# Kernel optimization log

Measured on AMD Instinct MI355X. Metric: run time of the kernel, lower is better.

Reference implementation:

```python
import jax, jax.numpy as jnp
import numpy as np

B, S, D, L, H = 2, 2048, 2048, 3, 16
DH = D // H
BLOCK = 16
NA = 64
Q = NA * BLOCK
KV = S + Q
VOCAB = 32000
MASK_ID = 31999
GAMMA = 7.0
EPS = 1e-6


def _rope(x, pos):
    # x: [B,H,T,DH], pos: [B,T]
    half = DH // 2
    inv = 1.0 / (10000.0 ** (jnp.arange(half, dtype=jnp.float32) / half))
    ang = pos[:, None, :, None].astype(jnp.float32) * inv  # [B,1,T,half]
    c, s = jnp.cos(ang), jnp.sin(ang)
    x1, x2 = x[..., :half], x[..., half:]
    return jnp.concatenate([x1 * c - x2 * s, x2 * c + x1 * s], axis=-1)


def setup_inputs() -> dict:
    key = jax.random.key(0)
    ks = jax.random.split(key, 12)
    w = lambda k, shp: 0.02 * jax.random.normal(k, shp, jnp.float32)
    return {
        'input_ids': jax.random.randint(ks[0], (B, S), 0, VOCAB, dtype=jnp.int32),
        'hidden_states': jax.random.normal(ks[1], (L, B, S, D), jnp.float32),
        'loss_mask': jnp.ones((B, S), jnp.int32),
        'lm_head_weight': w(ks[2], (VOCAB, D)),
        'norm_weight': jnp.ones((D,), jnp.float32),
        'anchor_positions': jnp.sort(jax.random.randint(ks[3], (B, NA), 0, S - BLOCK, dtype=jnp.int32), axis=-1),
        'ctx_proj_w': w(ks[4], (D, L * D)),
        'embed_table': w(ks[5], (VOCAB, D)),
        'wq': w(ks[6], (D, D)),
        'wk': w(ks[7], (D, D)),
        'wv': w(ks[8], (D, D)),
        'wo': w(ks[9], (D, D)),
    }


def reference(input_ids, hidden_states, loss_mask, lm_head_weight, norm_weight,
              anchor_positions, ctx_proj_w, embed_table, wq, wk, wv, wo):
    # --- context feature: concat L target-layer hiddens, project to D ---
    ctx_cat = jnp.transpose(hidden_states, (1, 2, 0, 3)).reshape(B, S, L * D)
    ctx = jnp.einsum('bsf,df->bsd', ctx_cat, ctx_proj_w)

    # --- position ids (context: 0..S-1; draft block i starts at anchor_i) ---
    ctx_pos = jnp.broadcast_to(jnp.arange(S, dtype=jnp.int32), (B, S))
    draft_pos = (anchor_positions[:, :, None] + jnp.arange(BLOCK, dtype=jnp.int32)[None, None, :]).reshape(B, Q)

    # --- draft input (anchor token + MASKs) and labels ---
    off = jnp.arange(Q, dtype=jnp.int32) % BLOCK                       # [Q]
    anchor_per_tok = jnp.repeat(anchor_positions, BLOCK, axis=1)       # [B,Q]
    anchor_tok = jnp.take_along_axis(input_ids, anchor_positions, axis=1)
    draft_ids = jnp.where(off[None, :] == 0, jnp.repeat(anchor_tok, BLOCK, axis=1), MASK_ID)
    labels = jnp.where(off[None, :] == 0, -100,
                       jnp.take_along_axis(input_ids, anchor_per_tok + off[None, :], axis=1))

    # --- block-causal mask: [B,Q,KV] ---
    qi = jnp.arange(Q, dtype=jnp.int32)
    ki = jnp.arange(KV, dtype=jnp.int32)
    qb = qi // BLOCK                                                   # [Q]
    apos = anchor_positions[:, qb]                                     # [B,Q]
    ctx_vis = (ki[None, None, :] < S) & (ki[None, None, :] < apos[:, :, None])
    kb = (ki - S) // BLOCK
    draft_vis = (ki >= S)[None, :] & (qb[:, None] == kb[None, :])      # [Q,KV]
    mask = ctx_vis | draft_vis[None]                                   # [B,Q,KV]

    # --- single RoPE attention layer: draft queries over [context; draft] ---
    emb = embed_table[draft_ids]                                       # [B,Q,D]
    x_kv = jnp.concatenate([ctx, emb], axis=1)                         # [B,KV,D]
    pos_kv = jnp.concatenate([ctx_pos, draft_pos], axis=1)             # [B,KV]
    q = _rope((emb @ wq.T).reshape(B, Q, H, DH).transpose(0, 2, 1, 3), draft_pos)
    k = _rope((x_kv @ wk.T).reshape(B, KV, H, DH).transpose(0, 2, 1, 3), pos_kv)
    v = (x_kv @ wv.T).reshape(B, KV, H, DH).transpose(0, 2, 1, 3)
    scores = jnp.einsum('bhqd,bhkd->bhqk', q, k) / np.float32(np.sqrt(DH))
    scores = jnp.where(mask[:, None], scores, jnp.float32(-1e30))
    attn = jax.nn.softmax(scores, axis=-1)
    out = jnp.einsum('bhqk,bhkd->bhqd', attn, v).transpose(0, 2, 1, 3).reshape(B, Q, D) @ wo.T
    hidden = emb + out

    # --- RMSNorm + LM head ---
    hidden = hidden * jax.lax.rsqrt(jnp.mean(hidden * hidden, -1, keepdims=True) + EPS) * norm_weight
    logits = hidden @ lm_head_weight.T                                 # [B,Q,VOCAB]

    # --- decay-weighted CE loss + accuracy ---
    logp = jax.nn.log_softmax(logits, axis=-1)
    lab = jnp.where(labels < 0, 0, labels)
    nll = -jnp.take_along_axis(logp, lab[..., None], axis=-1)[..., 0]
    valid = labels != -100
    offf = off.astype(jnp.float32)
    decay = jnp.where(off == 0, 0.0, jnp.exp(-(offf - 1.0) / GAMMA))   # [Q]
    w = decay[None, :] * valid.astype(jnp.float32)
    loss = jnp.sum(nll * w) / jnp.maximum(jnp.sum(w), 1e-6)
    preds = jnp.argmax(logits, axis=-1).astype(labels.dtype)
    acc = jnp.sum((preds == labels) & valid) / jnp.maximum(jnp.sum(valid), 1)
    return loss, acc.astype(jnp.float32)
```

## Files before the change

kernel.cpp:

```cpp
#include <hip/hip_runtime.h>

#define B_ 2
#define S_ 2048
#define D_ 2048
#define L_ 3
#define H_ 16
#define DH_ 128
#define BLK_ 16
#define NA_ 64
#define Q_ 1024
#define KV_ 3072
#define VOCAB_ 32000
#define MASK_ID_ 31999
#define NTOK_ (B_*Q_)
#define VTILES_ (VOCAB_/128)
#define NCHUNK_ 4

typedef __attribute__((ext_vector_type(8))) short bf16x8;
typedef __attribute__((ext_vector_type(4))) float f32x4;
typedef const __attribute__((address_space(1))) void* gptr_t;
typedef __attribute__((address_space(3))) void* lptr_t;

__device__ inline unsigned short f2bf(float x) {
  unsigned int u = __float_as_uint(x);
  unsigned int r = (u + 0x7fff + ((u >> 16) & 1)) >> 16;
  return (unsigned short)r;
}
__device__ inline float bf2f(unsigned short u) {
  return __uint_as_float(((unsigned int)u) << 16);
}

__global__ void k_meta(const int* __restrict__ ids, const int* __restrict__ anchors,
                       int* __restrict__ dids, int* __restrict__ dpos, int* __restrict__ labels) {
  int t = blockIdx.x * 256 + threadIdx.x;
  if (t >= NTOK_) return;
  int b = t >> 10, qi = t & 1023;
  int a = qi >> 4, off = qi & 15;
  int ap = anchors[b * NA_ + a];
  dpos[t] = ap + off;
  dids[t] = (off == 0) ? ids[b * S_ + ap] : MASK_ID_;
  labels[t] = (off == 0) ? -100 : ids[b * S_ + ap + off];
}

__global__ void k_cvt(const float* __restrict__ in, unsigned short* __restrict__ out, int n4) {
  int i = blockIdx.x * 256 + threadIdx.x;
  if (i >= n4) return;
  float4 v = ((const float4*)in)[i];
  ushort4 o;
  o.x = f2bf(v.x); o.y = f2bf(v.y); o.z = f2bf(v.z); o.w = f2bf(v.w);
  ((ushort4*)out)[i] = o;
}

__global__ void k_cvt_ctx(const float* __restrict__ hs, unsigned short* __restrict__ out) {
  int bi = blockIdx.x;
  int l = bi % 3, row = bi / 3;
  const float4* src = (const float4*)(hs + ((size_t)l * B_ * S_ + row) * (size_t)D_);
  ushort4* dst = (ushort4*)(out + (size_t)row * (3 * D_) + (size_t)l * D_);
  for (int i = threadIdx.x; i < D_ / 4; i += 256) {
    float4 v = src[i];
    ushort4 o;
    o.x = f2bf(v.x); o.y = f2bf(v.y); o.z = f2bf(v.z); o.w = f2bf(v.w);
    dst[i] = o;
  }
}

__global__ void k_gather(const float* __restrict__ table, const int* __restrict__ dids,
                         unsigned short* __restrict__ x_kv) {
  int row = blockIdx.x;
  int b = row >> 10, qi = row & 1023;
  const float4* src = (const float4*)(table + (size_t)dids[row] * D_);
  ushort4* dst = (ushort4*)(x_kv + ((size_t)b * KV_ + S_ + qi) * D_);
  for (int i = threadIdx.x; i < D_ / 4; i += 256) {
    float4 v = src[i];
    ushort4 o;
    o.x = f2bf(v.x); o.y = f2bf(v.y); o.z = f2bf(v.z); o.w = f2bf(v.w);
    dst[i] = o;
  }
}

template <int CMODE, int MAP>
__global__ __launch_bounds__(256) void k_mfma_bt(
    const unsigned short* __restrict__ A, const unsigned short* __restrict__ Bw,
    float* __restrict__ Cf, unsigned short* __restrict__ Cb,
    int M, int N, int K, int adivlog, long long abump, int cdivlog, long long cbump,
    const int* __restrict__ labels, float* __restrict__ pm, float* __restrict__ ps,
    int* __restrict__ pbi, float* __restrict__ plab) {
  __shared__ unsigned short As[128 * 32];
  __shared__ unsigned short Bs[128 * 32];
  int bx, by;
  if (MAP == 0) {
    int ntn = N >> 7;
    bx = blockIdx.x % ntn, by = blockIdx.x / ntn;
  } else {
    int per = gridDim.x >> 3;
    int wgid = (blockIdx.x & 7) * per + (blockIdx.x >> 3);
    int ntm = M >> 7;
    by = wgid % ntm, bx = wgid / ntm;
  }
  int rowbase = by << 7, colbase = bx << 7;
  int tid = threadIdx.x, lane = tid & 63, w = tid >> 6;
  int wr = w >> 1, wc = w & 1;
  int lo = lane & 15, hi = lane >> 4;

  f32x4 acc[4][4];
#pragma unroll
  for (int m = 0; m < 4; ++m)
#pragma unroll
    for (int n = 0; n < 4; ++n) acc[m][n] = (f32x4){0.f, 0.f, 0.f, 0.f};

  for (int kt = 0; kt < K; kt += 32) {
#pragma unroll
    for (int i = 0; i < 2; ++i) {
      int seg = i * 4 + w;
      int rloc = seg * 16 + (lane >> 2);
      int kcol = kt + ((lane & 3) << 3);
      int ra = rowbase + rloc;
      long long aoff = (long long)ra * K + (long long)(ra >> adivlog) * abump + kcol;
      __builtin_amdgcn_global_load_lds((gptr_t)(A + aoff), (lptr_t)(As + seg * 512), 16, 0, 0);
      int rb = colbase + rloc;
      long long boff = (long long)rb * K + kcol;
      __builtin_amdgcn_global_load_lds((gptr_t)(Bw + boff), (lptr_t)(Bs + seg * 512), 16, 0, 0);
    }
    __syncthreads();
    bf16x8 af[4], bfv[4];
#pragma unroll
    for (int m = 0; m < 4; ++m) {
      int row = wr * 64 + m * 16 + lo;
      af[m] = *(const bf16x8*)(As + row * 32 + (hi << 3));
    }
#pragma unroll
    for (int n = 0; n < 4; ++n) {
      int row = wc * 64 + n * 16 + lo;
      bfv[n] = *(const bf16x8*)(Bs + row * 32 + (hi << 3));
    }
#pragma unroll
    for (int m = 0; m < 4; ++m)
#pragma unroll
      for (int n = 0; n < 4; ++n)
        acc[m][n] = __builtin_amdgcn_mfma_f32_16x16x32_bf16(af[m], bfv[n], acc[m][n], 0, 0, 0);
    __syncthreads();
  }

  if (CMODE == 0 || CMODE == 1) {
#pragma unroll
    for (int m = 0; m < 4; ++m)
#pragma unroll
      for (int n = 0; n < 4; ++n)
#pragma unroll
        for (int r4 = 0; r4 < 4; ++r4) {
          int row = rowbase + wr * 64 + m * 16 + hi * 4 + r4;
          int col = colbase + wc * 64 + n * 16 + lo;
          size_t addr = (size_t)row * N + (size_t)(row >> cdivlog) * cbump + col;
          if (CMODE == 0) Cf[addr] = acc[m][n][r4];
          else Cb[addr] = f2bf(acc[m][n][r4]);
        }
  } else if (CMODE == 3) {
#pragma unroll
    for (int m = 0; m < 4; ++m)
#pragma unroll
      for (int n = 0; n < 4; ++n)
#pragma unroll
        for (int r4 = 0; r4 < 4; ++r4) {
          int row = rowbase + wr * 64 + m * 16 + hi * 4 + r4;
          int col = colbase + wc * 64 + n * 16 + lo;
          int bb = row >= KV_;
          int kv = row - bb * KV_;
          size_t addr = ((size_t)(bb * H_ + (col >> 7)) * 128 + (col & 127)) * KV_ + kv;
          Cb[addr] = f2bf(acc[m][n][r4]);
        }
  } else {
    float* f = (float*)As;
    int* ii = (int*)Bs;
    if (tid < 128) { f[640 + tid] = -3.0e38f; ii[256 + tid] = labels[rowbase + tid]; }
    __syncthreads();
#pragma unroll
    for (int m = 0; m < 4; ++m)
#pragma unroll
      for (int r4 = 0; r4 < 4; ++r4) {
        int trow = wr * 64 + m * 16 + hi * 4 + r4;
        float mx = acc[m][0][r4];
        int arg = colbase + wc * 64 + 0 * 16 + lo;
#pragma unroll
        for (int n = 1; n < 4; ++n) {
          float v = acc[m][n][r4];
          int c = colbase + wc * 64 + n * 16 + lo;
          if (v > mx || (v == mx && c < arg)) { mx = v; arg = c; }
        }
#pragma unroll
        for (int d = 1; d < 16; d <<= 1) {
          float om = __shfl_xor(mx, d);
          int oc = __shfl_xor(arg, d);
          if (om > mx || (om == mx && oc < arg)) { mx = om; arg = oc; }
        }
        if (lo == 0) { f[wc * 128 + trow] = mx; ii[wc * 128 + trow] = arg; }
      }
    __syncthreads();
    if (tid < 128) {
      float a = f[tid], b = f[128 + tid];
      int aa = ii[tid], bb = ii[128 + tid];
      float g; int ga;
      if (b > a || (b == a && bb < aa)) { g = b; ga = bb; } else { g = a; ga = aa; }
      f[512 + tid] = g; ii[384 + tid] = ga;
    }
    __syncthreads();
#pragma unroll
    for (int m = 0; m < 4; ++m)
#pragma unroll
      for (int r4 = 0; r4 < 4; ++r4) {
        int trow = wr * 64 + m * 16 + hi * 4 + r4;
        float gm = f[512 + trow];
        float s = 0.f;
#pragma unroll
        for (int n = 0; n < 4; ++n) s += __expf(acc[m][n][r4] - gm);
#pragma unroll
        for (int d = 1; d < 16; d <<= 1) s += __shfl_xor(s, d);
        if (lo == 0) f[256 + wc * 128 + trow] = s;
        int lab = ii[256 + trow];
        int rel = lab - colbase - wc * 64;
        if (rel >= 0 && rel < 64 && (rel & 15) == lo) {
#pragma unroll
          for (int n = 0; n < 4; ++n)
            if ((rel >> 4) == n) f[640 + trow] = acc[m][n][r4];
        }
      }
    __syncthreads();
    if (tid < 128) {
      int grow = rowbase + tid;
      size_t p = (size_t)grow * VTILES_ + bx;
      pm[p] = f[512 + tid];
      ps[p] = f[256 + tid] + f[256 + 128 + tid];
      pbi[p] = ii[384 + tid];
      plab[p] = f[640 + tid];
    }
  }
}

__global__ void k_rope(unsigned short* __restrict__ x, const int* __restrict__ dpos, int mode) {
  int idx = blockIdx.x * 256 + threadIdx.x;
  int j = idx & 63;
  int h = (idx >> 6) & 15;
  int row = idx >> 10;
  int pos;
  if (mode == 0) {
    if (row >= NTOK_) return;
    pos = dpos[row];
  } else {
    if (row >= B_ * KV_) return;
    int b = row / KV_, kvi = row % KV_;
    pos = (kvi < S_) ? kvi : dpos[b * Q_ + (kvi - S_)];
  }
  float inv = expf(-(float)j * (9.210340371976184f / 64.f));
  float ang = (float)pos * inv;
  float c = cosf(ang), s = sinf(ang);
  unsigned short* p = x + (size_t)row * D_ + h * DH_ + j;
  float x1 = bf2f(p[0]), x2 = bf2f(p[64]);
  p[0] = f2bf(x1 * c - x2 * s);
  p[64] = f2bf(x2 * c + x1 * s);
}

__global__ __launch_bounds__(256) void k_attn_part(
    const unsigned short* __restrict__ qb, const unsigned short* __restrict__ kb,
    const unsigned short* __restrict__ vt, const int* __restrict__ anchors,
    float* __restrict__ pm_att, float* __restrict__ pl_att, float* __restrict__ po_att) {
  __shared__ __align__(16) unsigned short P_all[4][16 * 40];
  int w = threadIdx.x >> 6, lane = threadIdx.x & 63;
  int blk = blockIdx.x * 4 + w;
  int chunk = blk & 3, h = (blk >> 2) & 15, a = (blk >> 6) & 63, b = blk >> 12;
  int ql = lane & 15, p = lane >> 4;
  int apos = anchors[b * NA_ + a];

  int cstart = chunk << 9;
  int cend = min(apos, cstart + 512);
  int len = (cend > cstart) ? (cend - cstart) : 0;
  int ntile = (len + 31) >> 5;
  int total = ntile + ((chunk == 3) ? 1 : 0);

  if (total == 0) {
    if (p == 0) { pm_att[blk * 16 + ql] = -3.0e38f; pl_att[blk * 16 + ql] = 0.f; }
    return;
  }
  unsigned short* P = P_all[w];

  const unsigned short* qbase = qb + ((size_t)(b * Q_ + a * 16 + ql)) * D_ + h * DH_;
  bf16x8 qf[4];
#pragma unroll
  for (int ks = 0; ks < 4; ++ks)
    qf[ks] = *(const bf16x8*)(qbase + ks * 32 + p * 8);

  const unsigned short* kbb = kb + (size_t)b * KV_ * D_ + h * DH_;
  const unsigned short* vtb = vt + ((size_t)(b * H_ + h)) * 128 * KV_;

  f32x4 o[8];
#pragma unroll
  for (int nt = 0; nt < 8; ++nt) o[nt] = (f32x4){0.f, 0.f, 0.f, 0.f};
  float mrun = -3.0e38f, lrun = 0.f;
  const float scl = 0.08838834764831845f;

  for (int t = 0; t < total; ++t) {
    bool isdraft = (chunk == 3) && (t == ntile);
    int ktb = isdraft ? (S_ + a * 16) : (cstart + (t << 5));
    int vc = isdraft ? 16 : min(32, cend - ktb);
    float s[2][4];
#pragma unroll
    for (int g = 0; g < 2; ++g) {
      if (g * 16 < vc) {
        f32x4 accs = (f32x4){0.f, 0.f, 0.f, 0.f};
        const unsigned short* krow = kbb + (size_t)(ktb + g * 16 + ql) * D_;
#pragma unroll
        for (int ks = 0; ks < 4; ++ks) {
          bf16x8 kf = *(const bf16x8*)(krow + ks * 32 + p * 8);
          accs = __builtin_amdgcn_mfma_f32_16x16x32_bf16(kf, qf[ks], accs, 0, 0, 0);
        }
#pragma unroll
        for (int r = 0; r < 4; ++r) {
          int kl = g * 16 + p * 4 + r;
          s[g][r] = (kl < vc) ? accs[r] * scl : -3.0e38f;
        }
      } else {
#pragma unroll
        for (int r = 0; r < 4; ++r) s[g][r] = -3.0e38f;
      }
    }
    float mt = s[0][0];
#pragma unroll
    for (int g = 0; g < 2; ++g)
#pragma unroll
      for (int r = 0; r < 4; ++r) mt = fmaxf(mt, s[g][r]);
    mt = fmaxf(mt, __shfl_xor(mt, 16));
    mt = fmaxf(mt, __shfl_xor(mt, 32));
    float mnew = fmaxf(mrun, mt);
    float corr = __expf(mrun - mnew);
    float psum = 0.f;
#pragma unroll
    for (int g = 0; g < 2; ++g) {
      float p0 = __expf(s[g][0] - mnew), p1 = __expf(s[g][1] - mnew);
      float p2 = __expf(s[g][2] - mnew), p3 = __expf(s[g][3] - mnew);
      psum += p0 + p1 + p2 + p3;
      ushort2 w0, w1;
      w0.x = f2bf(p0); w0.y = f2bf(p1); w1.x = f2bf(p2); w1.y = f2bf(p3);
      int eo = ql * 40 + g * 16 + p * 4;
      *(ushort2*)(P + eo) = w0;
      *(ushort2*)(P + eo + 2) = w1;
    }
    psum += __shfl_xor(psum, 16);
    psum += __shfl_xor(psum, 32);
    lrun = lrun * corr + psum;
    mrun = mnew;
    float cr[4];
#pragma unroll
    for (int r = 0; r < 4; ++r) cr[r] = __shfl(corr, p * 4 + r);
#pragma unroll
    for (int nt = 0; nt < 8; ++nt)
#pragma unroll
      for (int r = 0; r < 4; ++r) o[nt][r] *= cr[r];
    bf16x8 pf = *(const bf16x8*)(P + ql * 40 + p * 8);
#pragma unroll
    for (int nt = 0; nt < 8; ++nt) {
      bf16x8 vf = *(const bf16x8*)(vtb + (size_t)(nt * 16 + ql) * KV_ + ktb + p * 8);
      o[nt] = __builtin_amdgcn_mfma_f32_16x16x32_bf16(pf, vf, o[nt], 0, 0, 0);
    }
  }
  if (p == 0) { pm_att[blk * 16 + ql] = mrun; pl_att[blk * 16 + ql] = lrun; }
  float* pob = po_att + (size_t)blk * 2048;
#pragma unroll
  for (int nt = 0; nt < 8; ++nt)
#pragma unroll
    for (int r = 0; r < 4; ++r)
      pob[(p * 4 + r) * 128 + nt * 16 + ql] = o[nt][r];
}

__global__ __launch_bounds__(256) void k_attn_combine(
    const float* __restrict__ pm_att, const float* __restrict__ pl_att,
    const float* __restrict__ po_att, unsigned short* __restrict__ ob) {
  int base = blockIdx.x;
  int h = base & 15, a = (base >> 4) & 63, b = base >> 10;
  int d = threadIdx.x & 127, qh = threadIdx.x >> 7;
  int pbase = base * 4;
#pragma unroll
  for (int qq = 0; qq < 8; ++qq) {
    int q = qh * 8 + qq;
    float m0 = pm_att[(pbase + 0) * 16 + q], m1 = pm_att[(pbase + 1) * 16 + q];
    float m2 = pm_att[(pbase + 2) * 16 + q], m3 = pm_att[(pbase + 3) * 16 + q];
    float mg = fmaxf(fmaxf(m0, m1), fmaxf(m2, m3));
    float w0 = __expf(m0 - mg), w1 = __expf(m1 - mg);
    float w2 = __expf(m2 - mg), w3 = __expf(m3 - mg);
    float lg = pl_att[(pbase + 0) * 16 + q] * w0 + pl_att[(pbase + 1) * 16 + q] * w1 +
               pl_att[(pbase + 2) * 16 + q] * w2 + pl_att[(pbase + 3) * 16 + q] * w3;
    float od = po_att[(size_t)(pbase + 0) * 2048 + q * 128 + d] * w0 +
               po_att[(size_t)(pbase + 1) * 2048 + q * 128 + d] * w1 +
               po_att[(size_t)(pbase + 2) * 2048 + q * 128 + d] * w2 +
               po_att[(size_t)(pbase + 3) * 2048 + q * 128 + d] * w3;
    ob[((size_t)(b * Q_ + a * 16 + q)) * D_ + h * DH_ + d] = f2bf(od / lg);
  }
}

__global__ void k_rmsnorm(const unsigned short* __restrict__ x_kv, const float* __restrict__ proj,
                          const float* __restrict__ nw, unsigned short* __restrict__ outp) {
  int row = blockIdx.x;
  int b = row >> 10, qi = row & 1023;
  const unsigned short* emb = x_kv + ((size_t)b * KV_ + S_ + qi) * D_;
  const float* pr = proj + (size_t)row * D_;
  __shared__ float red[256];
  float h[8];
  float ssum = 0.f;
#pragma unroll
  for (int i = 0; i < 8; ++i) {
    int d = threadIdx.x + i * 256;
    h[i] = bf2f(emb[d]) + pr[d];
    ssum += h[i] * h[i];
  }
  red[threadIdx.x] = ssum;
  __syncthreads();
  for (int s = 128; s; s >>= 1) {
    if (threadIdx.x < s) red[threadIdx.x] += red[threadIdx.x + s];
    __syncthreads();
  }
  float scale = rsqrtf(red[0] / (float)D_ + 1e-6f);
#pragma unroll
  for (int i = 0; i < 8; ++i) {
    int d = threadIdx.x + i * 256;
    outp[(size_t)row * D_ + d] = f2bf(h[i] * scale * nw[d]);
  }
}

__global__ void k_combine(const float* __restrict__ pm, const float* __restrict__ ps,
                          const int* __restrict__ pbi, const float* __restrict__ plab,
                          const int* __restrict__ labels, float* __restrict__ ts) {
  int t = blockIdx.x * 256 + threadIdx.x;
  if (t >= NTOK_) return;
  const float* pmr = pm + (size_t)t * VTILES_;
  const float* psr = ps + (size_t)t * VTILES_;
  const int* pbir = pbi + (size_t)t * VTILES_;
  const float* plabr = plab + (size_t)t * VTILES_;
  float M = -3.0e38f; int bi = 0;
  for (int x = 0; x < VTILES_; ++x) {
    float v = pmr[x];
    if (v > M) { M = v; bi = pbir[x]; }
  }
  float ssum = 0.f, labl = -3.0e38f;
  for (int x = 0; x < VTILES_; ++x) {
    ssum += psr[x] * __expf(pmr[x] - M);
    labl = fmaxf(labl, plabr[x]);
  }
  float lse = M + logf(ssum);
  int lab = labels[t];
  int off = t & 15;
  float valid = (lab != -100) ? 1.f : 0.f;
  float w = (off == 0) ? 0.f : __expf(-(float)(off - 1) / 7.0f);
  w *= valid;
  float nll = (lab != -100) ? (lse - labl) : 0.f;
  float correct = (valid > 0.f && bi == lab) ? 1.f : 0.f;
  ts[t * 4 + 0] = nll * w;
  ts[t * 4 + 1] = w;
  ts[t * 4 + 2] = correct;
  ts[t * 4 + 3] = valid;
}

__global__ void k_finalize(const float* __restrict__ ts, float* __restrict__ out) {
  __shared__ float r0[256], r1[256], r2[256], r3[256];
  int tid = threadIdx.x;
  float s0 = 0, s1 = 0, s2 = 0, s3 = 0;
  for (int t = tid; t < NTOK_; t += 256) {
    s0 += ts[t * 4 + 0]; s1 += ts[t * 4 + 1];
    s2 += ts[t * 4 + 2]; s3 += ts[t * 4 + 3];
  }
  r0[tid] = s0; r1[tid] = s1; r2[tid] = s2; r3[tid] = s3;
  __syncthreads();
  for (int s = 128; s; s >>= 1) {
    if (tid < s) {
      r0[tid] += r0[tid + s]; r1[tid] += r1[tid + s];
      r2[tid] += r2[tid + s]; r3[tid] += r3[tid + s];
    }
    __syncthreads();
  }
  if (tid == 0) {
    out[0] = r0[0] / fmaxf(r1[0], 1e-6f);
    out[1] = r2[0] / fmaxf(r3[0], 1.f);
  }
}

extern "C" void kernel_launch(void* const* d_in, const int* in_sizes, int n_in,
                              void* d_out, int out_size, void* d_ws, size_t ws_size,
                              hipStream_t stream) {
  const int* input_ids = (const int*)d_in[0];
  const float* hs = (const float*)d_in[1];
  const float* lm_head = (const float*)d_in[3];
  const float* norm_w = (const float*)d_in[4];
  const int* anchors = (const int*)d_in[5];
  const float* ctx_w = (const float*)d_in[6];
  const float* embed = (const float*)d_in[7];
  const float* wq = (const float*)d_in[8];
  const float* wk = (const float*)d_in[9];
  const float* wv = (const float*)d_in[10];
  const float* wo = (const float*)d_in[11];
  float* out = (float*)d_out;

  char* base = (char*)d_ws;
  size_t off = 0;
  unsigned short* x_kv_bf = (unsigned short*)(base + off); off += (size_t)B_ * KV_ * D_ * 2;
  unsigned short* wkb = (unsigned short*)(base + off); off += (size_t)D_ * D_ * 2;
  unsigned short* wvb = (unsigned short*)(base + off); off += (size_t)D_ * D_ * 2;
  unsigned short* wqb = (unsigned short*)(base + off); off += (size_t)D_ * D_ * 2;
  unsigned short* wob = (unsigned short*)(base + off); off += (size_t)D_ * D_ * 2;
  unsigned short* hidden_bf = (unsigned short*)(base + off); off += (size_t)NTOK_ * D_ * 2;
  unsigned short* attn_bf = (unsigned short*)(base + off); off += (size_t)NTOK_ * D_ * 2;
  float* proj = (float*)(base + off); off += (size_t)NTOK_ * D_ * 4;
  float* pm = (float*)(base + off); off += (size_t)NTOK_ * VTILES_ * 4;
  float* psum = (float*)(base + off); off += (size_t)NTOK_ * VTILES_ * 4;
  float* plab = (float*)(base + off); off += (size_t)NTOK_ * VTILES_ * 4;
  int* pbi = (int*)(base + off); off += (size_t)NTOK_ * VTILES_ * 4;
  float* tstats = (float*)(base + off); off += (size_t)NTOK_ * 4 * 4;
  int* dids = (int*)(base + off); off += NTOK_ * 4;
  int* dpos = (int*)(base + off); off += NTOK_ * 4;
  int* labels = (int*)(base + off); off += NTOK_ * 4;
  char* regA = base + off;
  const size_t SLACK = 65536;
  unsigned short* ctxA = (unsigned short*)(regA);
  unsigned short* ctx_wbf = (unsigned short*)(regA + 50331648);
  unsigned short* kbuf = (unsigned short*)(regA + 50331648 + 25165824);
  unsigned short* vtbuf = (unsigned short*)(regA + 50331648 + 2 * 25165824 + SLACK);
  unsigned short* qbuf = (unsigned short*)(regA + 50331648 + 3 * 25165824 + 2 * SLACK);
  unsigned short* lm_bf = (unsigned short*)(regA);
  float* po_att = (float*)(regA);
  float* pm_att = (float*)(regA + 67108864);
  float* pl_att = (float*)(regA + 67108864 + 524288);

  k_meta<<<(NTOK_ + 255) / 256, 256, 0, stream>>>(input_ids, anchors, dids, dpos, labels);
  k_cvt<<<((D_ * (L_ * D_) / 4) + 255) / 256, 256, 0, stream>>>(ctx_w, ctx_wbf, D_ * (L_ * D_) / 4);
  k_cvt<<<((D_ * D_ / 4) + 255) / 256, 256, 0, stream>>>(wk, wkb, D_ * D_ / 4);
  k_cvt<<<((D_ * D_ / 4) + 255) / 256, 256, 0, stream>>>(wv, wvb, D_ * D_ / 4);
  k_cvt<<<((D_ * D_ / 4) + 255) / 256, 256, 0, stream>>>(wq, wqb, D_ * D_ / 4);
  k_cvt<<<((D_ * D_ / 4) + 255) / 256, 256, 0, stream>>>(wo, wob, D_ * D_ / 4);
  k_cvt_ctx<<<B_ * S_ * L_, 256, 0, stream>>>(hs, ctxA);
  k_gather<<<NTOK_, 256, 0, stream>>>(embed, dids, x_kv_bf);

  k_mfma_bt<1, 0><<<(4096 / 128) * (2048 / 128), 256, 0, stream>>>(
      ctxA, ctx_wbf, nullptr, x_kv_bf, 4096, 2048, 6144, 30, 0LL, 11, (long long)Q_ * D_,
      nullptr, nullptr, nullptr, nullptr, nullptr);
  k_mfma_bt<1, 0><<<(6144 / 128) * (2048 / 128), 256, 0, stream>>>(
      x_kv_bf, wkb, nullptr, kbuf, 6144, 2048, 2048, 30, 0LL, 30, 0LL,
      nullptr, nullptr, nullptr, nullptr, nullptr);
  k_mfma_bt<3, 0><<<(6144 / 128) * (2048 / 128), 256, 0, stream>>>(
      x_kv_bf, wvb, nullptr, vtbuf, 6144, 2048, 2048, 30, 0LL, 30, 0LL,
      nullptr, nullptr, nullptr, nullptr, nullptr);
  k_mfma_bt<1, 0><<<(2048 / 128) * (2048 / 128), 256, 0, stream>>>(
      x_kv_bf + (size_t)S_ * D_, wqb, nullptr, qbuf, 2048, 2048, 2048, 10,
      (long long)(KV_ - Q_) * D_, 30, 0LL,
      nullptr, nullptr, nullptr, nullptr, nullptr);
  k_rope<<<(NTOK_ * H_ * 64) / 256, 256, 0, stream>>>(qbuf, dpos, 0);
  k_rope<<<(B_ * KV_ * H_ * 64) / 256, 256, 0, stream>>>(kbuf, dpos, 1);
  k_attn_part<<<(B_ * NA_ * H_ * NCHUNK_) / 4, 256, 0, stream>>>(
      qbuf, kbuf, vtbuf, anchors, pm_att, pl_att, po_att);
  k_attn_combine<<<B_ * NA_ * H_, 256, 0, stream>>>(pm_att, pl_att, po_att, attn_bf);
  k_mfma_bt<0, 0><<<(2048 / 128) * (2048 / 128), 256, 0, stream>>>(
      attn_bf, wob, proj, nullptr, 2048, 2048, 2048, 30, 0LL, 30, 0LL,
      nullptr, nullptr, nullptr, nullptr, nullptr);
  k_rmsnorm<<<NTOK_, 256, 0, stream>>>(x_kv_bf, proj, norm_w, hidden_bf);
  k_cvt<<<((VOCAB_ * D_ / 4) + 255) / 256, 256, 0, stream>>>(lm_head, lm_bf, VOCAB_ * D_ / 4);
  k_mfma_bt<2, 1><<<(2048 / 128) * (VOCAB_ / 128), 256, 0, stream>>>(
      hidden_bf, lm_bf, nullptr, nullptr, 2048, VOCAB_, 2048, 30, 0LL, 30, 0LL,
      labels, pm, psum, pbi, plab);
  k_combine<<<(NTOK_ + 255) / 256, 256, 0, stream>>>(pm, psum, pbi, plab, labels, tstats);
  k_finalize<<<1, 256, 0, stream>>>(tstats, out);
}
```

Baseline: 1.312 ms.

## Add triple-buffered direct-to-LDS GEMM kernel with 128x256 tiles for most projections

Introduces k_gemm3, a 512-thread GEMM with 128x256 output tiles, BK=64, and a 3-stage LDS ring filled by global_load_lds with XOR-swizzled layout. It uses explicit vmcnt waits so loads for future stages overlap the MFMA work. All projections except the V-transpose, plus the fused LM-head cross-entropy epilogue, are switched to it, which halves the number of per-token partial vocab tiles. It targets the global-load latency and bank conflicts of the old single-buffered 128x128 kernel, at the cost of roughly 144KB of LDS (one block per CU) and fewer blocks for the smaller GEMMs.

```diff
diff --git a/kernel.cpp b/kernel.cpp
--- a/kernel.cpp
+++ b/kernel.cpp
@@ -13,7 +13,7 @@
 #define VOCAB_ 32000
 #define MASK_ID_ 31999
 #define NTOK_ (B_*Q_)
-#define VTILES_ (VOCAB_/128)
+#define VT2_ (VOCAB_/256)
 #define NCHUNK_ 4
 
 typedef __attribute__((ext_vector_type(8))) short bf16x8;
@@ -78,25 +78,205 @@
   }
 }
 
-template <int CMODE, int MAP>
-__global__ __launch_bounds__(256) void k_mfma_bt(
+#define STAGE3(s_, kt_)                                                        \
+  {                                                                            \
+    unsigned short* as_ = &Asl[s_][0];                                         \
+    unsigned short* bs_ = &Bsl[s_][0];                                         \
+    _Pragma("unroll")                                                          \
+    for (int i_ = 0; i_ < 2; ++i_)                                             \
+      __builtin_amdgcn_global_load_lds((gptr_t)(A + aoff[i_] + (kt_)),         \
+          (lptr_t)((char*)as_ + adst[i_]), 16, 0, 0);                          \
+    _Pragma("unroll")                                                          \
+    for (int i_ = 0; i_ < 4; ++i_)                                             \
+      __builtin_amdgcn_global_load_lds((gptr_t)(Bw + boff[i_] + (kt_)),        \
+          (lptr_t)((char*)bs_ + bdst[i_]), 16, 0, 0);                          \
+  }
+
+template <int CMODE>
+__global__ __launch_bounds__(512, 1) void k_gemm3(
     const unsigned short* __restrict__ A, const unsigned short* __restrict__ Bw,
     float* __restrict__ Cf, unsigned short* __restrict__ Cb,
     int M, int N, int K, int adivlog, long long abump, int cdivlog, long long cbump,
     const int* __restrict__ labels, float* __restrict__ pm, float* __restrict__ ps,
     int* __restrict__ pbi, float* __restrict__ plab) {
+  __shared__ unsigned short Asl[3][128 * 64];
+  __shared__ unsigned short Bsl[3][256 * 64];
+  int ntm = M >> 7;
+  int per = gridDim.x >> 3;
+  int wgid = (blockIdx.x & 7) * per + (blockIdx.x >> 3);
+  int by = wgid % ntm, bx = wgid / ntm;
+  int rowbase = by << 7, colbase = bx << 8;
+  int tid = threadIdx.x, l = tid & 63, w = tid >> 6;
+  int wm = w >> 2, wn = w & 3;
+  int lo = l & 15, hi = l >> 4;
+
+  long long aoff[2]; int adst[2];
+#pragma unroll
+  for (int i = 0; i < 2; ++i) {
+    int rl = w * 16 + i * 8 + (l >> 3);
+    int cu = (l & 7) ^ (rl & 7);
+    long long ra = rowbase + rl;
+    aoff[i] = ra * K + (ra >> adivlog) * abump + cu * 8;
+    adst[i] = (w * 128 + i * 64) * 16;
+  }
+  long long boff[4]; int bdst[4];
+#pragma unroll
+  for (int i = 0; i < 4; ++i) {
+    int rl = w * 32 + i * 8 + (l >> 3);
+    int cu = (l & 7) ^ (rl & 7);
+    long long rb = colbase + rl;
+    boff[i] = rb * K + cu * 8;
+    bdst[i] = (w * 256 + i * 64) * 16;
+  }
+  int ard[4][2], brd[4][2];
+#pragma unroll
+  for (int m = 0; m < 4; ++m)
+#pragma unroll
+    for (int ks = 0; ks < 2; ++ks) {
+      int row = wm * 64 + m * 16 + lo;
+      int pos = ((ks << 2) | hi) ^ (row & 7);
+      ard[m][ks] = row * 64 + pos * 8;
+      row = wn * 64 + m * 16 + lo;
+      pos = ((ks << 2) | hi) ^ (row & 7);
+      brd[m][ks] = row * 64 + pos * 8;
+    }
+
+  f32x4 acc[4][4];
+#pragma unroll
+  for (int m = 0; m < 4; ++m)
+#pragma unroll
+    for (int n = 0; n < 4; ++n) acc[m][n] = (f32x4){0.f, 0.f, 0.f, 0.f};
+
+  int NT = K >> 6;
+  STAGE3(0, 0);
+  STAGE3(1, 64);
+  STAGE3(2, 128);
+
+  int s = 0;
+  for (int t = 0; t < NT; ++t) {
+    if (t < NT - 2)       asm volatile("s_waitcnt vmcnt(12)" ::: "memory");
+    else if (t == NT - 2) asm volatile("s_waitcnt vmcnt(6)" ::: "memory");
+    else                  asm volatile("s_waitcnt vmcnt(0)" ::: "memory");
+    __builtin_amdgcn_s_barrier();
+    asm volatile("" ::: "memory");
+    const unsigned short* as_ = &Asl[s][0];
+    const unsigned short* bs_ = &Bsl[s][0];
+    bf16x8 af[4][2], bg[4][2];
+#pragma unroll
+    for (int m = 0; m < 4; ++m)
+#pragma unroll
+      for (int ks = 0; ks < 2; ++ks) {
+        af[m][ks] = *(const bf16x8*)(as_ + ard[m][ks]);
+        bg[m][ks] = *(const bf16x8*)(bs_ + brd[m][ks]);
+      }
+    __builtin_amdgcn_s_setprio(1);
+#pragma unroll
+    for (int m = 0; m < 4; ++m)
+#pragma unroll
+      for (int n = 0; n < 4; ++n) {
+        acc[m][n] = __builtin_amdgcn_mfma_f32_16x16x32_bf16(af[m][0], bg[n][0], acc[m][n], 0, 0, 0);
+        acc[m][n] = __builtin_amdgcn_mfma_f32_16x16x32_bf16(af[m][1], bg[n][1], acc[m][n], 0, 0, 0);
+      }
+    __builtin_amdgcn_s_setprio(0);
+    __builtin_amdgcn_sched_barrier(0);
+    asm volatile("" ::: "memory");
+    __builtin_amdgcn_s_barrier();
+    if (t + 3 < NT) STAGE3(s, (t + 3) << 6);
+    s = (s == 2) ? 0 : s + 1;
+  }
+
+  if (CMODE == 0 || CMODE == 1) {
+#pragma unroll
+    for (int m = 0; m < 4; ++m)
+#pragma unroll
+      for (int n = 0; n < 4; ++n)
+#pragma unroll
+        for (int r4 = 0; r4 < 4; ++r4) {
+          int row = rowbase + wm * 64 + m * 16 + hi * 4 + r4;
+          int col = colbase + wn * 64 + n * 16 + lo;
+          size_t addr = (size_t)row * N + (size_t)(row >> cdivlog) * cbump + col;
+          if (CMODE == 0) Cf[addr] = acc[m][n][r4];
+          else Cb[addr] = f2bf(acc[m][n][r4]);
+        }
+  } else {
+    float* f = (float*)&Asl[0][0];
+    int* ii = (int*)&Bsl[0][0];
+    if (tid < 128) { f[1152 + tid] = -3.0e38f; ii[640 + tid] = labels[rowbase + tid]; }
+    __syncthreads();
+#pragma unroll
+    for (int m = 0; m < 4; ++m)
+#pragma unroll
+      for (int r4 = 0; r4 < 4; ++r4) {
+        int rl = wm * 64 + m * 16 + hi * 4 + r4;
+        float mx = acc[m][0][r4];
+        int arg = colbase + wn * 64 + lo;
+#pragma unroll
+        for (int n = 1; n < 4; ++n) {
+          float v = acc[m][n][r4];
+          int c = colbase + wn * 64 + n * 16 + lo;
+          if (v > mx) { mx = v; arg = c; }
+        }
+#pragma unroll
+        for (int d = 1; d < 16; d <<= 1) {
+          float om = __shfl_xor(mx, d);
+          int oc = __shfl_xor(arg, d);
+          if (om > mx || (om == mx && oc < arg)) { mx = om; arg = oc; }
+        }
+        if (lo == 0) { f[wn * 128 + rl] = mx; ii[wn * 128 + rl] = arg; }
+      }
+    __syncthreads();
+    if (tid < 128) {
+      float m0 = f[tid]; int a0 = ii[tid];
+#pragma unroll
+      for (int x = 1; x < 4; ++x) {
+        float v = f[x * 128 + tid]; int c = ii[x * 128 + tid];
+        if (v > m0 || (v == m0 && c < a0)) { m0 = v; a0 = c; }
+      }
+      f[1024 + tid] = m0; ii[512 + tid] = a0;
+    }
+    __syncthreads();
+#pragma unroll
+    for (int m = 0; m < 4; ++m)
+#pragma unroll
+      for (int r4 = 0; r4 < 4; ++r4) {
+        int rl = wm * 64 + m * 16 + hi * 4 + r4;
+        float gm = f[1024 + rl];
+        float sacc = 0.f;
+#pragma unroll
+        for (int n = 0; n < 4; ++n) sacc += __expf(acc[m][n][r4] - gm);
+#pragma unroll
+        for (int d = 1; d < 16; d <<= 1) sacc += __shfl_xor(sacc, d);
+        if (lo == 0) f[512 + wn * 128 + rl] = sacc;
+        int lab = ii[640 + rl];
+        int rel = lab - colbase;
+        if (rel >= 0 && rel < 256 && (rel >> 6) == wn && (rel & 15) == lo) {
+          int n_own = (rel >> 4) & 3;
+#pragma unroll
+          for (int n = 0; n < 4; ++n)
+            if (n == n_own) f[1152 + rl] = acc[m][n][r4];
+        }
+      }
+    __syncthreads();
+    if (tid < 128) {
+      int grow = rowbase + tid;
+      size_t p = (size_t)grow * VT2_ + bx;
+      pm[p] = f[1024 + tid];
+      ps[p] = f[512 + tid] + f[512 + 128 + tid] + f[512 + 256 + tid] + f[512 + 384 + tid];
+      pbi[p] = ii[512 + tid];
+      plab[p] = f[1152 + tid];
+    }
+  }
+}
+
+template <int CMODE, int MAP>
+__global__ __launch_bounds__(256) void k_mfma_bt(
+    const unsigned short* __restrict__ A, const unsigned short* __restrict__ Bw,
+    float* __restrict__ Cf, unsigned short* __restrict__ Cb,
+    int M, int N, int K, int adivlog, long long abump, int cdivlog, long long cbump) {
   __shared__ unsigned short As[128 * 32];
   __shared__ unsigned short Bs[128 * 32];
-  int bx, by;
-  if (MAP == 0) {
-    int ntn = N >> 7;
-    bx = blockIdx.x % ntn, by = blockIdx.x / ntn;
-  } else {
-    int per = gridDim.x >> 3;
-    int wgid = (blockIdx.x & 7) * per + (blockIdx.x >> 3);
-    int ntm = M >> 7;
-    by = wgid % ntm, bx = wgid / ntm;
-  }
+  int ntn = N >> 7;
+  int bx = blockIdx.x % ntn, by = blockIdx.x / ntn;
   int rowbase = by << 7, colbase = bx << 7;
   int tid = threadIdx.x, lane = tid & 63, w = tid >> 6;
   int wr = w >> 1, wc = w & 1;
@@ -140,99 +320,19 @@
         acc[m][n] = __builtin_amdgcn_mfma_f32_16x16x32_bf16(af[m], bfv[n], acc[m][n], 0, 0, 0);
     __syncthreads();
   }
-
-  if (CMODE == 0 || CMODE == 1) {
-#pragma unroll
-    for (int m = 0; m < 4; ++m)
-#pragma unroll
-      for (int n = 0; n < 4; ++n)
-#pragma unroll
-        for (int r4 = 0; r4 < 4; ++r4) {
-          int row = rowbase + wr * 64 + m * 16 + hi * 4 + r4;
-          int col = colbase + wc * 64 + n * 16 + lo;
-          size_t addr = (size_t)row * N + (size_t)(row >> cdivlog) * cbump + col;
-          if (CMODE == 0) Cf[addr] = acc[m][n][r4];
-          else Cb[addr] = f2bf(acc[m][n][r4]);
-        }
-  } else if (CMODE == 3) {
-#pragma unroll
-    for (int m = 0; m < 4; ++m)
-#pragma unroll
-      for (int n = 0; n < 4; ++n)
-#pragma unroll
-        for (int r4 = 0; r4 < 4; ++r4) {
-          int row = rowbase + wr * 64 + m * 16 + hi * 4 + r4;
-          int col = colbase + wc * 64 + n * 16 + lo;
-          int bb = row >= KV_;
-          int kv = row - bb * KV_;
-          size_t addr = ((size_t)(bb * H_ + (col >> 7)) * 128 + (col & 127)) * KV_ + kv;
-          Cb[addr] = f2bf(acc[m][n][r4]);
-        }
-  } else {
-    float* f = (float*)As;
-    int* ii = (int*)Bs;
-    if (tid < 128) { f[640 + tid] = -3.0e38f; ii[256 + tid] = labels[rowbase + tid]; }
-    __syncthreads();
-#pragma unroll
-    for (int m = 0; m < 4; ++m)
+#pragma unroll
+  for (int m = 0; m < 4; ++m)
+#pragma unroll
+    for (int n = 0; n < 4; ++n)
 #pragma unroll
       for (int r4 = 0; r4 < 4; ++r4) {
-        int trow = wr * 64 + m * 16 + hi * 4 + r4;
-        float mx = acc[m][0][r4];
-        int arg = colbase + wc * 64 + 0 * 16 + lo;
-#pragma unroll
-        for (int n = 1; n < 4; ++n) {
-          float v = acc[m][n][r4];
-          int c = colbase + wc * 64 + n * 16 + lo;
-          if (v > mx || (v == mx && c < arg)) { mx = v; arg = c; }
-        }
-#pragma unroll
-        for (int d = 1; d < 16; d <<= 1) {
-          float om = __shfl_xor(mx, d);
-          int oc = __shfl_xor(arg, d);
-          if (om > mx || (om == mx && oc < arg)) { mx = om; arg = oc; }
-        }
-        if (lo == 0) { f[wc * 128 + trow] = mx; ii[wc * 128 + trow] = arg; }
+        int row = rowbase + wr * 64 + m * 16 + hi * 4 + r4;
+        int col = colbase + wc * 64 + n * 16 + lo;
+        int bb = row >= KV_;
+        int kv = row - bb * KV_;
+        size_t addr = ((size_t)(bb * H_ + (col >> 7)) * 128 + (col & 127)) * KV_ + kv;
+        Cb[addr] = f2bf(acc[m][n][r4]);
       }
-    __syncthreads();
-    if (tid < 128) {
-      float a = f[tid], b = f[128 + tid];
-      int aa = ii[tid], bb = ii[128 + tid];
-      float g; int ga;
-      if (b > a || (b == a && bb < aa)) { g = b; ga = bb; } else { g = a; ga = aa; }
-      f[512 + tid] = g; ii[384 + tid] = ga;
-    }
-    __syncthreads();
-#pragma unroll
-    for (int m = 0; m < 4; ++m)
-#pragma unroll
-      for (int r4 = 0; r4 < 4; ++r4) {
-        int trow = wr * 64 + m * 16 + hi * 4 + r4;
-        float gm = f[512 + trow];
-        float s = 0.f;
-#pragma unroll
-        for (int n = 0; n < 4; ++n) s += __expf(acc[m][n][r4] - gm);
-#pragma unroll
-        for (int d = 1; d < 16; d <<= 1) s += __shfl_xor(s, d);
-        if (lo == 0) f[256 + wc * 128 + trow] = s;
-        int lab = ii[256 + trow];
-        int rel = lab - colbase - wc * 64;
-        if (rel >= 0 && rel < 64 && (rel & 15) == lo) {
-#pragma unroll
-          for (int n = 0; n < 4; ++n)
-            if ((rel >> 4) == n) f[640 + trow] = acc[m][n][r4];
-        }
-      }
-    __syncthreads();
-    if (tid < 128) {
-      int grow = rowbase + tid;
-      size_t p = (size_t)grow * VTILES_ + bx;
-      pm[p] = f[512 + tid];
-      ps[p] = f[256 + tid] + f[256 + 128 + tid];
-      pbi[p] = ii[384 + tid];
-      plab[p] = f[640 + tid];
-    }
-  }
 }
 
 __global__ void k_rope(unsigned short* __restrict__ x, const int* __restrict__ dpos, int mode) {
@@ -428,17 +528,17 @@
                           const int* __restrict__ labels, float* __restrict__ ts) {
   int t = blockIdx.x * 256 + threadIdx.x;
   if (t >= NTOK_) return;
-  const float* pmr = pm + (size_t)t * VTILES_;
-  const float* psr = ps + (size_t)t * VTILES_;
-  const int* pbir = pbi + (size_t)t * VTILES_;
-  const float* plabr = plab + (size_t)t * VTILES_;
+  const float* pmr = pm + (size_t)t * VT2_;
+  const float* psr = ps + (size_t)t * VT2_;
+  const int* pbir = pbi + (size_t)t * VT2_;
+  const float* plabr = plab + (size_t)t * VT2_;
   float M = -3.0e38f; int bi = 0;
-  for (int x = 0; x < VTILES_; ++x) {
+  for (int x = 0; x < VT2_; ++x) {
     float v = pmr[x];
     if (v > M) { M = v; bi = pbir[x]; }
   }
   float ssum = 0.f, labl = -3.0e38f;
-  for (int x = 0; x < VTILES_; ++x) {
+  for (int x = 0; x < VT2_; ++x) {
     ssum += psr[x] * __expf(pmr[x] - M);
     labl = fmaxf(labl, plabr[x]);
   }
@@ -505,10 +605,10 @@
   unsigned short* hidden_bf = (unsigned short*)(base + off); off += (size_t)NTOK_ * D_ * 2;
   unsigned short* attn_bf = (unsigned short*)(base + off); off += (size_t)NTOK_ * D_ * 2;
   float* proj = (float*)(base + off); off += (size_t)NTOK_ * D_ * 4;
-  float* pm = (float*)(base + off); off += (size_t)NTOK_ * VTILES_ * 4;
-  float* psum = (float*)(base + off); off += (size_t)NTOK_ * VTILES_ * 4;
-  float* plab = (float*)(base + off); off += (size_t)NTOK_ * VTILES_ * 4;
-  int* pbi = (int*)(base + off); off += (size_t)NTOK_ * VTILES_ * 4;
+  float* pm = (float*)(base + off); off += (size_t)NTOK_ * 250 * 4;
+  float* psum = (float*)(base + off); off += (size_t)NTOK_ * 250 * 4;
+  float* plab = (float*)(base + off); off += (size_t)NTOK_ * 250 * 4;
+  int* pbi = (int*)(base + off); off += (size_t)NTOK_ * 250 * 4;
   float* tstats = (float*)(base + off); off += (size_t)NTOK_ * 4 * 4;
   int* dids = (int*)(base + off); off += NTOK_ * 4;
   int* dpos = (int*)(base + off); off += NTOK_ * 4;
@@ -534,16 +634,15 @@
   k_cvt_ctx<<<B_ * S_ * L_, 256, 0, stream>>>(hs, ctxA);
   k_gather<<<NTOK_, 256, 0, stream>>>(embed, dids, x_kv_bf);
 
-  k_mfma_bt<1, 0><<<(4096 / 128) * (2048 / 128), 256, 0, stream>>>(
+  k_gemm3<1><<<(4096 / 128) * (2048 / 256), 512, 0, stream>>>(
       ctxA, ctx_wbf, nullptr, x_kv_bf, 4096, 2048, 6144, 30, 0LL, 11, (long long)Q_ * D_,
       nullptr, nullptr, nullptr, nullptr, nullptr);
-  k_mfma_bt<1, 0><<<(6144 / 128) * (2048 / 128), 256, 0, stream>>>(
+  k_gemm3<1><<<(6144 / 128) * (2048 / 256), 512, 0, stream>>>(
       x_kv_bf, wkb, nullptr, kbuf, 6144, 2048, 2048, 30, 0LL, 30, 0LL,
       nullptr, nullptr, nullptr, nullptr, nullptr);
   k_mfma_bt<3, 0><<<(6144 / 128) * (2048 / 128), 256, 0, stream>>>(
-      x_kv_bf, wvb, nullptr, vtbuf, 6144, 2048, 2048, 30, 0LL, 30, 0LL,
-      nullptr, nullptr, nullptr, nullptr, nullptr);
-  k_mfma_bt<1, 0><<<(2048 / 128) * (2048 / 128), 256, 0, stream>>>(
+      x_kv_bf, wvb, nullptr, vtbuf, 6144, 2048, 2048, 30, 0LL, 30, 0LL);
+  k_gemm3<1><<<(2048 / 128) * (2048 / 256), 512, 0, stream>>>(
       x_kv_bf + (size_t)S_ * D_, wqb, nullptr, qbuf, 2048, 2048, 2048, 10,
       (long long)(KV_ - Q_) * D_, 30, 0LL,
       nullptr, nullptr, nullptr, nullptr, nullptr);
@@ -552,12 +651,12 @@
   k_attn_part<<<(B_ * NA_ * H_ * NCHUNK_) / 4, 256, 0, stream>>>(
       qbuf, kbuf, vtbuf, anchors, pm_att, pl_att, po_att);
   k_attn_combine<<<B_ * NA_ * H_, 256, 0, stream>>>(pm_att, pl_att, po_att, attn_bf);
-  k_mfma_bt<0, 0><<<(2048 / 128) * (2048 / 128), 256, 0, stream>>>(
+  k_gemm3<0><<<(2048 / 128) * (2048 / 256), 512, 0, stream>>>(
       attn_bf, wob, proj, nullptr, 2048, 2048, 2048, 30, 0LL, 30, 0LL,
       nullptr, nullptr, nullptr, nullptr, nullptr);
   k_rmsnorm<<<NTOK_, 256, 0, stream>>>(x_kv_bf, proj, norm_w, hidden_bf);
   k_cvt<<<((VOCAB_ * D_ / 4) + 255) / 256, 256, 0, stream>>>(lm_head, lm_bf, VOCAB_ * D_ / 4);
-  k_mfma_bt<2, 1><<<(2048 / 128) * (VOCAB_ / 128), 256, 0, stream>>>(
+  k_gemm3<2><<<(2048 / 128) * (VOCAB_ / 256), 512, 0, stream>>>(
       hidden_bf, lm_bf, nullptr, nullptr, 2048, VOCAB_, 2048, 30, 0LL, 30, 0LL,
       labels, pm, psum, pbi, plab);
   k_combine<<<(NTOK_ + 255) / 256, 256, 0, stream>>>(pm, psum, pbi, plab, labels, tstats);
```

New measurement: 1.346 ms. 2.6% more time.
